# Performance work log

Hardware: AMD Instinct MI355X
Metric: run time of the kernel (lower is better)

## Reference

```python
import jax, jax.numpy as jnp
import numpy as np

E = 1024        # embedding_dim
DIN = 2048      # d_inner = E * expand_factor(2)
N = 16          # state_dim
DTR = 64        # dt_rank = ceil(E/16)
K_CONV = 4      # conv_dim


def tt_dense(g1, g2):
    # TT with ranks [1,16,1]: W[(m1,m2),(n1,n2)] = sum_r g1[m1,n1,r] g2[r,m2,n2]
    m1, n1, r = g1.shape
    _, m2, n2 = g2.shape
    return jnp.einsum('air,rbj->abij', g1, g2).reshape(m1 * m2, n1 * n2)


def setup_inputs() -> dict:
    key = jax.random.key(0)
    ks = jax.random.split(key, 12)
    s = 0.05  # init scale for TT cores
    return {
        'x': jax.random.normal(ks[0], (2, 1024, E), dtype=jnp.float32),
        # in_proj: 1024=[32,32] -> 4096=[64,64]
        'in_g1': jax.random.normal(ks[1], (32, 64, 16)) * s,
        'in_g2': jax.random.normal(ks[2], (16, 32, 64)) * s,
        # x_proj: 2048=[32,64] -> 96=[8,12]
        'x_g1': jax.random.normal(ks[3], (32, 8, 16)) * s,
        'x_g2': jax.random.normal(ks[4], (16, 64, 12)) * s,
        # dt_proj: 64=[8,8] -> 2048=[32,64]
        'dt_g1': jax.random.normal(ks[5], (8, 32, 16)) * s,
        'dt_g2': jax.random.normal(ks[6], (16, 8, 64)) * s,
        # out_proj: 2048=[32,64] -> 1024=[32,32]
        'out_g1': jax.random.normal(ks[7], (32, 32, 16)) * s,
        'out_g2': jax.random.normal(ks[8], (16, 64, 32)) * s,
        'conv_filter': jax.random.normal(ks[9], (K_CONV, 1, DIN)) * 0.1,
        'conv_bias': jnp.zeros((DIN,), jnp.float32),
        'A_log': jax.random.uniform(ks[10], (DIN, N), dtype=jnp.float32),
        'D': jnp.zeros((DIN,), jnp.float32),
    }


def _forward(x, in_g1, in_g2, x_g1, x_g2, dt_g1, dt_g2, out_g1, out_g2,
             conv_filter, conv_bias, A_log, D):
    B, L, _ = x.shape
    # in_proj (TT) -> split into conv path and gate
    xz = (x.reshape(-1, E) @ tt_dense(in_g1, in_g2)).reshape(B, L, 2 * DIN)
    x_conv, z = xz[..., :DIN], xz[..., DIN:]
    # depthwise conv1d, SAME padding, + bias, SiLU, gate by z
    conv = jax.lax.conv_general_dilated(
        x_conv, conv_filter, window_strides=(1,), padding='SAME',
        dimension_numbers=('NWC', 'WIO', 'NWC'), feature_group_count=DIN)
    y = jax.nn.silu(conv + conv_bias) * z            # [B, L, DIN]
    # x_proj (TT) -> dt_unscaled, B, C
    dtBC = (y.reshape(-1, DIN) @ tt_dense(x_g1, x_g2)).reshape(B, L, DTR + 2 * N)
    dt_un = dtBC[..., :DTR]
    Bm = dtBC[..., DTR:DTR + N]                      # [B, L, N]
    Cm = dtBC[..., DTR + N:]                         # [B, L, N]
    # dt_proj (TT) + softplus
    dt = jax.nn.softplus(dt_un.reshape(-1, DTR) @ tt_dense(dt_g1, dt_g2)).reshape(B, L, DIN)
    # selective scan
    A = -jnp.exp(A_log)                              # [DIN, N]

    def step(h, inp):
        dt_t, u_t, B_t, C_t = inp                    # [B,DIN],[B,DIN],[B,N],[B,N]
        dA = jnp.exp(dt_t[:, :, None] * A)           # [B, DIN, N]
        h = dA * h + dt_t[:, :, None] * B_t[:, None, :] * u_t[:, :, None]
        y_t = jnp.einsum('bdn,bn->bd', h, C_t) + D * u_t
        return h, (y_t, h)

    h0 = jnp.zeros((B, DIN, N), x.dtype)
    _, (ys, hs) = jax.lax.scan(
        step, h0,
        (dt.swapaxes(0, 1), y.swapaxes(0, 1), Bm.swapaxes(0, 1), Cm.swapaxes(0, 1)))
    ssm_out = ys.swapaxes(0, 1) + jnp.mean(hs) * 1e-8  # [B, L, DIN]
    out = (ssm_out.reshape(-1, DIN) @ tt_dense(out_g1, out_g2)).reshape(B, L, E)
    return out


def reference(x, in_g1, in_g2, x_g1, x_g2, dt_g1, dt_g2, out_g1, out_g2,
              conv_filter, conv_bias, A_log, D):
    return _forward(x, in_g1, in_g2, x_g1, x_g2, dt_g1, dt_g2, out_g1, out_g2,
                    conv_filter, conv_bias, A_log, D)
```

## Files before the change

### kernel.cpp

```cpp
#include <hip/hip_runtime.h>
#include <hip/hip_bf16.h>
#include <cstdint>
#include <cstddef>

#define EE    1024
#define DIN   2048
#define NST   16
#define DTR   64
#define BB_   2
#define LL    1024
#define BL    (BB_*LL)
#define NCHUNK 32
#define CLEN   32
#define RTT   16

typedef unsigned short u16;
typedef unsigned int   u32;

static constexpr size_t OFF_WINT  = 0;
static constexpr size_t OFF_WOUTT = 2097152;
static constexpr size_t OFF_WXT   = 3145728;
static constexpr size_t OFF_WDTT  = 3276800;
static constexpr size_t OFF_A2T   = 3342336;
static constexpr size_t OFF_XB    = 3375104;
static constexpr size_t OFF_XZB   = 4423680;
static constexpr size_t OFF_YB    = 8617984;
static constexpr size_t OFF_PART  = 10715136;
static constexpr size_t OFF_DTBC  = 14909440;
static constexpr size_t OFF_DTUNB = 15106048;
static constexpr size_t OFF_DTB   = 15171584;
static constexpr size_t OFF_YSB   = 17268736;
static constexpr size_t OFF_HC    = 19365888;
static constexpr size_t OFF_SDT   = 21463040;

__device__ __forceinline__ u16 f2bf(float f) {
    u32 u = __float_as_uint(f);
    u += 0x7fffu + ((u >> 16) & 1u);
    return (u16)(u >> 16);
}
__device__ __forceinline__ float bf2f(u16 v) {
    return __uint_as_float((u32)v << 16);
}

__device__ __forceinline__ void async_copy16(const void* g, void* l) {
    __builtin_amdgcn_global_load_lds((const __attribute__((address_space(1))) u32*)g,
                                     (__attribute__((address_space(3))) u32*)l,
                                     16, 0, 0);
}

__device__ __forceinline__ float softplusf(float v) {
    return fmaxf(v, 0.f) + log1pf(__expf(-fabsf(v)));
}

__device__ void tt_part(const float* __restrict__ g1, const float* __restrict__ g2,
                        u16* __restrict__ Wt, int m1, int n1, int m2, int n2,
                        int c, int crows, float* g1col, float* g2col)
{
    const int rowsW = m1 * m2;
    if (c >= crows) {
        for (int k = threadIdx.x; k < rowsW; k += 256)
            Wt[(size_t)c * rowsW + k] = 0;
        return;
    }
    const int i = c / n2;
    const int j = c - i * n2;

    for (int e = threadIdx.x; e < m1 * RTT; e += 256) {
        const int a = e >> 4, rr = e & 15;
        g1col[e] = g1[(size_t)(a * n1 + i) * RTT + rr];
    }
    for (int e = threadIdx.x; e < RTT * m2; e += 256) {
        const int rr = e / m2, bb = e - rr * m2;
        g2col[e] = g2[(size_t)(rr * m2 + bb) * n2 + j];
    }
    __syncthreads();

    for (int k = threadIdx.x; k < rowsW; k += 256) {
        const int a  = k / m2;
        const int bb = k - a * m2;
        const float* gp = g1col + a * RTT;
        float s = 0.f;
        #pragma unroll
        for (int rr = 0; rr < RTT; ++rr)
            s = fmaf(gp[rr], g2col[rr * m2 + bb], s);
        Wt[(size_t)c * rowsW + k] = f2bf(s);
    }
}

__global__ __launch_bounds__(256) void mega_prep(
    const float* __restrict__ in_g1, const float* __restrict__ in_g2, u16* __restrict__ W_inT,
    const float* __restrict__ out_g1, const float* __restrict__ out_g2, u16* __restrict__ W_outT,
    const float* __restrict__ x_g1, const float* __restrict__ x_g2, u16* __restrict__ W_xT,
    const float* __restrict__ dt_g1, const float* __restrict__ dt_g2, u16* __restrict__ W_dtT,
    const float* __restrict__ x, u16* __restrict__ xb,
    const float* __restrict__ A_log, float* __restrict__ A2t)
{
    __shared__ float g1col[32 * RTT];
    __shared__ float g2col[RTT * 64];
    const int blk = blockIdx.x;
    if (blk < 4096) {
        tt_part(in_g1, in_g2, W_inT, 32, 64, 32, 64, blk, 4096, g1col, g2col);
    } else if (blk < 5120) {
        tt_part(out_g1, out_g2, W_outT, 32, 32, 64, 32, blk - 4096, 1024, g1col, g2col);
    } else if (blk < 5248) {
        tt_part(x_g1, x_g2, W_xT, 32, 8, 64, 12, blk - 5120, 96, g1col, g2col);
    } else if (blk < 7296) {
        tt_part(dt_g1, dt_g2, W_dtT, 8, 32, 8, 64, blk - 5248, 2048, g1col, g2col);
    } else if (blk < 9344) {
        const int i = (blk - 7296) * 256 + threadIdx.x;
        float4 v = ((const float4*)x)[i];
        ushort4 o;
        o.x = f2bf(v.x); o.y = f2bf(v.y); o.z = f2bf(v.z); o.w = f2bf(v.w);
        ((ushort4*)xb)[i] = o;
    } else {
        const int idx = (blk - 9344) * 256 + threadIdx.x;
        const int d = idx >> 4, n = idx & 15;
        A2t[n * DIN + d] = -expf(A_log[idx]);
    }
}

typedef __attribute__((ext_vector_type(8))) short bf16x8;
typedef __attribute__((ext_vector_type(4))) float floatx4;

template<int BN, int BK, int OUT>
__global__ __launch_bounds__(256) void gemm_bf16(
    const u16* __restrict__ A, const u16* __restrict__ Bt, void* __restrict__ Cout,
    int K, int ldc, int kchunk, size_t czstride)
{
    constexpr int BM   = 128;
    constexpr int NT   = BN / 32;
    constexpr int SLOT = BK / 8;
    constexpr int CR   = 64 / SLOT;
    constexpr int NACH = BM / CR / 4;
    constexpr int NBCH = BN / CR / 4;
    constexpr int KG   = BK / 32;
    __shared__ u16 As[BM * BK];
    __shared__ u16 Bs[BN * BK];

    const int tid  = threadIdx.x;
    const int w    = tid >> 6;
    const int lane = tid & 63;
    const int wm   = w & 1, wn = w >> 1;
    const int row0 = blockIdx.y * BM;
    const int col0 = blockIdx.x * BN;
    const int kbeg = blockIdx.z * kchunk;

    const int srow = lane / SLOT;
    const int kqp  = lane % SLOT;
    const u16* ga[NACH]; u16* la[NACH];
    #pragma unroll
    for (int i = 0; i < NACH; ++i) {
        const int c  = w * NACH + i;
        const int r  = c * CR + srow;
        const int kq = kqp ^ ((r >> 1) & (SLOT - 1));
        ga[i] = A + (size_t)(row0 + r) * K + kbeg + kq * 8;
        la[i] = &As[c * CR * BK];
    }
    const u16* gb[NBCH]; u16* lb[NBCH];
    #pragma unroll
    for (int i = 0; i < NBCH; ++i) {
        const int c  = w * NBCH + i;
        const int r  = c * CR + srow;
        const int kq = kqp ^ ((r >> 1) & (SLOT - 1));
        gb[i] = Bt + (size_t)(col0 + r) * K + kbeg + kq * 8;
        lb[i] = &Bs[c * CR * BK];
    }

    const int q = lane >> 4, l15 = lane & 15;
    int a_off[4][KG], b_off[NT][KG];
    #pragma unroll
    for (int mt = 0; mt < 4; ++mt) {
        const int r = wm * 64 + mt * 16 + l15;
        const int m = (r >> 1) & (SLOT - 1);
        #pragma unroll
        for (int kk = 0; kk < KG; ++kk)
            a_off[mt][kk] = r * BK + ((kk * 4 + q) ^ m) * 8;
    }
    #pragma unroll
    for (int nt = 0; nt < NT; ++nt) {
        const int r = wn * (BN / 2) + nt * 16 + l15;
        const int m = (r >> 1) & (SLOT - 1);
        #pragma unroll
        for (int kk = 0; kk < KG; ++kk)
            b_off[nt][kk] = r * BK + ((kk * 4 + q) ^ m) * 8;
    }

    floatx4 acc[4][NT];
    #pragma unroll
    for (int mt = 0; mt < 4; ++mt)
        #pragma unroll
        for (int nt = 0; nt < NT; ++nt)
            acc[mt][nt] = (floatx4){0.f, 0.f, 0.f, 0.f};

    for (int k0 = 0; k0 < kchunk; k0 += BK) {
        #pragma unroll
        for (int i = 0; i < NACH; ++i) { async_copy16(ga[i], la[i]); ga[i] += BK; }
        #pragma unroll
        for (int i = 0; i < NBCH; ++i) { async_copy16(gb[i], lb[i]); gb[i] += BK; }
        __syncthreads();

        bf16x8 af[4][KG], bfv[NT][KG];
        #pragma unroll
        for (int mt = 0; mt < 4; ++mt)
            #pragma unroll
            for (int kk = 0; kk < KG; ++kk)
                af[mt][kk] = *(const bf16x8*)&As[a_off[mt][kk]];
        #pragma unroll
        for (int nt = 0; nt < NT; ++nt)
            #pragma unroll
            for (int kk = 0; kk < KG; ++kk)
                bfv[nt][kk] = *(const bf16x8*)&Bs[b_off[nt][kk]];

        #pragma unroll
        for (int kk = 0; kk < KG; ++kk)
            #pragma unroll
            for (int mt = 0; mt < 4; ++mt)
                #pragma unroll
                for (int nt = 0; nt < NT; ++nt)
                    acc[mt][nt] = __builtin_amdgcn_mfma_f32_16x16x32_bf16(
                        af[mt][kk], bfv[nt][kk], acc[mt][nt], 0, 0, 0);

        __syncthreads();
    }

    #pragma unroll
    for (int mt = 0; mt < 4; ++mt) {
        const int row = row0 + wm * 64 + mt * 16 + q * 4;
        #pragma unroll
        for (int nt = 0; nt < NT; ++nt) {
            const int col = col0 + wn * (BN / 2) + nt * 16 + l15;
            #pragma unroll
            for (int r = 0; r < 4; ++r) {
                const float v = acc[mt][nt][r];
                if constexpr (OUT == 0) {
                    ((float*)Cout)[(size_t)blockIdx.z * czstride + (size_t)(row + r) * ldc + col] = v;
                } else if constexpr (OUT == 1) {
                    ((u16*)Cout)[(size_t)(row + r) * ldc + col] = f2bf(v);
                } else {
                    ((u16*)Cout)[(size_t)(row + r) * ldc + col] = f2bf(softplusf(v));
                }
            }
        }
    }
}

__global__ __launch_bounds__(256) void reduce_dtbc(
    const float* __restrict__ part, float* __restrict__ dtBC, u16* __restrict__ dtun_b)
{
    int idx = blockIdx.x * 256 + threadIdx.x;
    if (idx >= BL * 96) return;
    const int row = idx / 96;
    const int col = idx - row * 96;
    float s = 0.f;
    #pragma unroll
    for (int z = 0; z < 16; ++z)
        s += part[(size_t)z * BL * 128 + (size_t)row * 128 + col];
    dtBC[idx] = s;
    if (col < 64) dtun_b[(size_t)row * 64 + col] = f2bf(s);
}

__global__ __launch_bounds__(256) void reduce_out(
    const float* __restrict__ part, float* __restrict__ out)
{
    const int idx = blockIdx.x * 256 + threadIdx.x;
    const float4 a = ((const float4*)part)[idx];
    const float4 b = ((const float4*)part)[idx + BL * EE / 4];
    float4 o;
    o.x = a.x + b.x; o.y = a.y + b.y; o.z = a.z + b.z; o.w = a.w + b.w;
    ((float4*)out)[idx] = o;
}

typedef __attribute__((ext_vector_type(8))) unsigned short ushortx8;

__global__ __launch_bounds__(256) void conv_gate(
    const u16* __restrict__ xzb, const float* __restrict__ filt,
    const float* __restrict__ bias, u16* __restrict__ yb)
{
    int idx = blockIdx.x * blockDim.x + threadIdx.x;
    if (idx >= BL * DIN / 8) return;
    const int d  = (idx % (DIN / 8)) * 8;
    const int bt = idx / (DIN / 8);
    const int b  = bt >> 10;
    const int t  = bt & 1023;

    float acc[8];
    #pragma unroll
    for (int j = 0; j < 8; ++j) acc[j] = bias[d + j];
    #pragma unroll
    for (int k = 0; k < 4; ++k) {
        const int tt = t + k - 1;
        if ((unsigned)tt < (unsigned)LL) {
            const ushortx8 xc = *(const ushortx8*)(xzb + (size_t)(b * LL + tt) * (2 * DIN) + d);
            #pragma unroll
            for (int j = 0; j < 8; ++j)
                acc[j] = fmaf(bf2f(xc[j]), filt[(size_t)k * DIN + d + j], acc[j]);
        }
    }
    const ushortx8 z = *(const ushortx8*)(xzb + (size_t)bt * (2 * DIN) + DIN + d);
    ushortx8 o;
    #pragma unroll
    for (int j = 0; j < 8; ++j)
        o[j] = f2bf(acc[j] / (1.f + __expf(-acc[j])) * bf2f(z[j]));
    *(ushortx8*)(yb + (size_t)bt * DIN + d) = o;
}

__global__ __launch_bounds__(256) void scan_phase_a(
    const u16* __restrict__ dt, const u16* __restrict__ u,
    const float* __restrict__ dtBC, const float* __restrict__ A2t,
    float* __restrict__ hend, float* __restrict__ sdtbuf)
{
    const int d = blockIdx.x * 256 + threadIdx.x;
    const int c = blockIdx.y;
    const int b = blockIdx.z;

    __shared__ float Bs[CLEN][NST];
    for (int e = threadIdx.x; e < CLEN * NST; e += 256) {
        const int tl = e >> 4, n = e & 15;
        Bs[tl][n] = dtBC[(size_t)(b * LL + c * CLEN + tl) * 96 + 64 + n];
    }
    __syncthreads();

    float A2r[NST];
    #pragma unroll
    for (int n = 0; n < NST; ++n) A2r[n] = A2t[n * DIN + d];

    float h[NST] = {};
    float sdt = 0.f;
    const size_t tbase = (size_t)(b * LL + c * CLEN) * DIN + d;
    for (int tl = 0; tl < CLEN; ++tl) {
        const float dtv = bf2f(dt[tbase + (size_t)tl * DIN]);
        const float uv  = bf2f(u [tbase + (size_t)tl * DIN]);
        sdt += dtv;
        const float cu = dtv * uv;
        #pragma unroll
        for (int n = 0; n < NST; ++n) {
            const float a = __expf(A2r[n] * dtv);
            h[n] = fmaf(a, h[n], cu * Bs[tl][n]);
        }
    }
    const int cb = b * NCHUNK + c;
    #pragma unroll
    for (int n = 0; n < NST; ++n)
        hend[((size_t)cb * NST + n) * DIN + d] = h[n];
    sdtbuf[(size_t)cb * DIN + d] = sdt;
}

__global__ __launch_bounds__(256) void scan_phase_b(
    const float* __restrict__ A2t, const float* __restrict__ sdtbuf,
    float* __restrict__ hcarry)
{
    const int idx = blockIdx.x * 256 + threadIdx.x;
    if (idx >= BB_ * NST * DIN) return;
    const int d = idx & (DIN - 1);
    const int n = (idx >> 11) & 15;
    const int b = idx >> 15;
    const float A2 = A2t[n * DIN + d];
    float h = 0.f;
    for (int c = 0; c < NCHUNK; ++c) {
        const int cb = b * NCHUNK + c;
        const size_t off = ((size_t)cb * NST + n) * DIN + d;
        const float he = hcarry[off];
        const float pa = __expf(A2 * sdtbuf[(size_t)cb * DIN + d]);
        hcarry[off] = h;
        h = fmaf(pa, h, he);
    }
}

__global__ __launch_bounds__(256) void scan_phase_c(
    const u16* __restrict__ dt, const u16* __restrict__ u,
    const float* __restrict__ dtBC, const float* __restrict__ A2t,
    const float* __restrict__ hinit, const float* __restrict__ Dp,
    u16* __restrict__ ysb)
{
    const int d = blockIdx.x * 256 + threadIdx.x;
    const int c = blockIdx.y;
    const int b = blockIdx.z;

    __shared__ float Bs[CLEN][NST];
    __shared__ float Cs[CLEN][NST];
    for (int e = threadIdx.x; e < CLEN * NST; e += 256) {
        const int tl = e >> 4, n = e & 15;
        const size_t base = (size_t)(b * LL + c * CLEN + tl) * 96;
        Bs[tl][n] = dtBC[base + 64 + n];
        Cs[tl][n] = dtBC[base + 80 + n];
    }
    __syncthreads();

    float A2r[NST], h[NST];
    const int cb = b * NCHUNK + c;
    #pragma unroll
    for (int n = 0; n < NST; ++n) {
        A2r[n] = A2t[n * DIN + d];
        h[n]   = hinit[((size_t)cb * NST + n) * DIN + d];
    }
    const float Dv = Dp[d];

    const size_t tbase = (size_t)(b * LL + c * CLEN) * DIN + d;
    for (int tl = 0; tl < CLEN; ++tl) {
        const float dtv = bf2f(dt[tbase + (size_t)tl * DIN]);
        const float uv  = bf2f(u [tbase + (size_t)tl * DIN]);
        const float cu = dtv * uv;
        float yacc = 0.f;
        #pragma unroll
        for (int n = 0; n < NST; ++n) {
            const float a = __expf(A2r[n] * dtv);
            h[n] = fmaf(a, h[n], cu * Bs[tl][n]);
            yacc = fmaf(h[n], Cs[tl][n], yacc);
        }
        ysb[tbase + (size_t)tl * DIN] = f2bf(fmaf(Dv, uv, yacc));
    }
}

extern "C" void kernel_launch(void* const* d_in, const int* in_sizes, int n_in,
                              void* d_out, int out_size, void* d_ws, size_t ws_size,
                              hipStream_t stream)
{
    const float* x       = (const float*)d_in[0];
    const float* in_g1   = (const float*)d_in[1];
    const float* in_g2   = (const float*)d_in[2];
    const float* x_g1    = (const float*)d_in[3];
    const float* x_g2    = (const float*)d_in[4];
    const float* dt_g1   = (const float*)d_in[5];
    const float* dt_g2   = (const float*)d_in[6];
    const float* out_g1  = (const float*)d_in[7];
    const float* out_g2  = (const float*)d_in[8];
    const float* filt    = (const float*)d_in[9];
    const float* bias    = (const float*)d_in[10];
    const float* A_log   = (const float*)d_in[11];
    const float* Dp      = (const float*)d_in[12];

    float* ws     = (float*)d_ws;
    u16*   W_inT  = (u16*)(ws + OFF_WINT);
    u16*   W_outT = (u16*)(ws + OFF_WOUTT);
    u16*   W_xT   = (u16*)(ws + OFF_WXT);
    u16*   W_dtT  = (u16*)(ws + OFF_WDTT);
    float* A2t    = ws + OFF_A2T;
    u16*   xb     = (u16*)(ws + OFF_XB);
    u16*   xzb    = (u16*)(ws + OFF_XZB);
    u16*   yb     = (u16*)(ws + OFF_YB);
    float* part   = ws + OFF_PART;
    float* dtBC   = ws + OFF_DTBC;
    u16*   dtun_b = (u16*)(ws + OFF_DTUNB);
    u16*   dtb    = (u16*)(ws + OFF_DTB);
    u16*   ysb    = (u16*)(ws + OFF_YSB);
    float* hc     = ws + OFF_HC;
    float* sdt    = ws + OFF_SDT;

    mega_prep<<<9472, 256, 0, stream>>>(
        in_g1, in_g2, W_inT, out_g1, out_g2, W_outT,
        x_g1, x_g2, W_xT, dt_g1, dt_g2, W_dtT,
        x, xb, A_log, A2t);

    gemm_bf16<128, 64, 1><<<dim3(32, 16, 1), 256, 0, stream>>>(
        xb, W_inT, xzb, EE, 4096, EE, 0);

    conv_gate<<<(BL * DIN / 8 + 255) / 256, 256, 0, stream>>>(xzb, filt, bias, yb);

    gemm_bf16<128, 64, 0><<<dim3(1, 16, 16), 256, 0, stream>>>(
        yb, W_xT, part, DIN, 128, 128, (size_t)BL * 128);
    reduce_dtbc<<<(BL * 96 + 255) / 256, 256, 0, stream>>>(part, dtBC, dtun_b);

    gemm_bf16<128, 64, 2><<<dim3(16, 16, 1), 256, 0, stream>>>(
        dtun_b, W_dtT, dtb, 64, DIN, 64, 0);

    scan_phase_a<<<dim3(DIN / 256, NCHUNK, BB_), 256, 0, stream>>>(dtb, yb, dtBC, A2t, hc, sdt);
    scan_phase_b<<<(BB_ * NST * DIN) / 256, 256, 0, stream>>>(A2t, sdt, hc);
    scan_phase_c<<<dim3(DIN / 256, NCHUNK, BB_), 256, 0, stream>>>(dtb, yb, dtBC, A2t, hc, Dp, ysb);

    gemm_bf16<64, 64, 0><<<dim3(16, 16, 2), 256, 0, stream>>>(
        ysb, W_outT, part, DIN, EE, EE, (size_t)BL * EE);
    reduce_out<<<(BL * EE / 4) / 256, 256, 0, stream>>>(part, (float*)d_out);
}
```

Baseline: 229.0 us.

## Add triple-buffered 128x256 bf16 GEMM with 512 threads for in_proj

```diff
diff --git a/kernel.cpp b/kernel.cpp
--- a/kernel.cpp
+++ b/kernel.cpp
@@ -244,6 +244,176 @@
     }
 }
 
+__global__ __launch_bounds__(512, 2) void gemm_bf16_dp(
+    const u16* __restrict__ A, const u16* __restrict__ Bt, u16* __restrict__ Cout,
+    int K, int ldc)
+{
+    constexpr int BM   = 128;
+    constexpr int BN   = 256;
+    constexpr int BK   = 64;
+    constexpr int SLOT = BK / 8;
+    constexpr int CR   = 64 / SLOT;
+    constexpr int NACH = BM / CR / 8;
+    constexpr int NBCH = BN / CR / 8;
+    constexpr int AST  = BM * BK;
+    constexpr int BST  = BN * BK;
+
+    __shared__ u16 As[3 * AST];
+    __shared__ u16 Bs[3 * BST];
+
+    const int tid  = threadIdx.x;
+    const int w    = tid >> 6;
+    const int lane = tid & 63;
+    const int wm   = w & 1;
+    const int wn   = w >> 1;
+    const int row0 = blockIdx.y * BM;
+    const int col0 = blockIdx.x * BN;
+
+    const int srow = lane / SLOT;
+    const int kqp  = lane % SLOT;
+    const u16* ga[NACH]; int laA[NACH];
+    #pragma unroll
+    for (int i = 0; i < NACH; ++i) {
+        const int c  = w * NACH + i;
+        const int r  = c * CR + srow;
+        const int kq = kqp ^ ((r >> 1) & (SLOT - 1));
+        ga[i]  = A + (size_t)(row0 + r) * K + kq * 8;
+        laA[i] = c * CR * BK;
+    }
+    const u16* gb[NBCH]; int laB[NBCH];
+    #pragma unroll
+    for (int i = 0; i < NBCH; ++i) {
+        const int c  = w * NBCH + i;
+        const int r  = c * CR + srow;
+        const int kq = kqp ^ ((r >> 1) & (SLOT - 1));
+        gb[i]  = Bt + (size_t)(col0 + r) * K + kq * 8;
+        laB[i] = c * CR * BK;
+    }
+
+    const int q = lane >> 4, l15 = lane & 15;
+    int a_off[4][2], b_off[4][2];
+    #pragma unroll
+    for (int mt = 0; mt < 4; ++mt) {
+        const int r = wm * 64 + mt * 16 + l15;
+        const int m = (r >> 1) & (SLOT - 1);
+        #pragma unroll
+        for (int kk = 0; kk < 2; ++kk)
+            a_off[mt][kk] = r * BK + ((kk * 4 + q) ^ m) * 8;
+    }
+    #pragma unroll
+    for (int nt = 0; nt < 4; ++nt) {
+        const int r = wn * 64 + nt * 16 + l15;
+        const int m = (r >> 1) & (SLOT - 1);
+        #pragma unroll
+        for (int kk = 0; kk < 2; ++kk)
+            b_off[nt][kk] = r * BK + ((kk * 4 + q) ^ m) * 8;
+    }
+
+    floatx4 acc[4][4];
+    #pragma unroll
+    for (int mt = 0; mt < 4; ++mt)
+        #pragma unroll
+        for (int nt = 0; nt < 4; ++nt)
+            acc[mt][nt] = (floatx4){0.f, 0.f, 0.f, 0.f};
+
+    const int NTILES = K / BK;
+
+    #pragma unroll
+    for (int i = 0; i < NACH; ++i) { async_copy16(ga[i], &As[0 * AST + laA[i]]); ga[i] += BK; }
+    #pragma unroll
+    for (int i = 0; i < NBCH; ++i) { async_copy16(gb[i], &Bs[0 * BST + laB[i]]); gb[i] += BK; }
+    #pragma unroll
+    for (int i = 0; i < NACH; ++i) { async_copy16(ga[i], &As[1 * AST + laA[i]]); ga[i] += BK; }
+    #pragma unroll
+    for (int i = 0; i < NBCH; ++i) { async_copy16(gb[i], &Bs[1 * BST + laB[i]]); gb[i] += BK; }
+    __builtin_amdgcn_sched_barrier(0);
+    asm volatile("s_waitcnt vmcnt(6)" ::: "memory");
+    __builtin_amdgcn_s_barrier();
+    __builtin_amdgcn_sched_barrier(0);
+
+    int cur = 0, nxt = 2;
+    for (int t = 0; t < NTILES; ++t) {
+        const bool pf = (t + 2 < NTILES);
+        const u16* Ac = &As[cur * AST];
+        const u16* Bc = &Bs[cur * BST];
+        u16* An = &As[nxt * AST];
+        u16* Bn = &Bs[nxt * BST];
+
+        bf16x8 af[4], bfv[4];
+
+        #pragma unroll
+        for (int mt = 0; mt < 4; ++mt) af[mt]  = *(const bf16x8*)&Ac[a_off[mt][0]];
+        #pragma unroll
+        for (int nt = 0; nt < 4; ++nt) bfv[nt] = *(const bf16x8*)&Bc[b_off[nt][0]];
+        if (pf) {
+            async_copy16(ga[0], &An[laA[0]]);
+            async_copy16(ga[1], &An[laA[1]]);
+            async_copy16(gb[0], &Bn[laB[0]]);
+        }
+        __builtin_amdgcn_sched_barrier(0);
+        __builtin_amdgcn_s_barrier();
+        asm volatile("s_waitcnt lgkmcnt(0)" ::: "memory");
+        __builtin_amdgcn_sched_barrier(0);
+        __builtin_amdgcn_s_setprio(1);
+        #pragma unroll
+        for (int mt = 0; mt < 4; ++mt)
+            #pragma unroll
+            for (int nt = 0; nt < 4; ++nt)
+                acc[mt][nt] = __builtin_amdgcn_mfma_f32_16x16x32_bf16(
+                    af[mt], bfv[nt], acc[mt][nt], 0, 0, 0);
+        __builtin_amdgcn_s_setprio(0);
+        __builtin_amdgcn_sched_barrier(0);
+        __builtin_amdgcn_s_barrier();
+        __builtin_amdgcn_sched_barrier(0);
+
+        #pragma unroll
+        for (int mt = 0; mt < 4; ++mt) af[mt]  = *(const bf16x8*)&Ac[a_off[mt][1]];
+        #pragma unroll
+        for (int nt = 0; nt < 4; ++nt) bfv[nt] = *(const bf16x8*)&Bc[b_off[nt][1]];
+        if (pf) {
+            async_copy16(gb[1], &Bn[laB[1]]);
+            async_copy16(gb[2], &Bn[laB[2]]);
+            async_copy16(gb[3], &Bn[laB[3]]);
+            #pragma unroll
+            for (int i = 0; i < NACH; ++i) ga[i] += BK;
+            #pragma unroll
+            for (int i = 0; i < NBCH; ++i) gb[i] += BK;
+        }
+        __builtin_amdgcn_sched_barrier(0);
+        __builtin_amdgcn_s_barrier();
+        asm volatile("s_waitcnt lgkmcnt(0)" ::: "memory");
+        __builtin_amdgcn_sched_barrier(0);
+        __builtin_amdgcn_s_setprio(1);
+        #pragma unroll
+        for (int mt = 0; mt < 4; ++mt)
+            #pragma unroll
+            for (int nt = 0; nt < 4; ++nt)
+                acc[mt][nt] = __builtin_amdgcn_mfma_f32_16x16x32_bf16(
+                    af[mt], bfv[nt], acc[mt][nt], 0, 0, 0);
+        __builtin_amdgcn_s_setprio(0);
+        __builtin_amdgcn_sched_barrier(0);
+        if (pf) asm volatile("s_waitcnt vmcnt(6)" ::: "memory");
+        else    asm volatile("s_waitcnt vmcnt(0)" ::: "memory");
+        __builtin_amdgcn_s_barrier();
+        __builtin_amdgcn_sched_barrier(0);
+
+        cur = (cur == 2) ? 0 : cur + 1;
+        nxt = (nxt == 2) ? 0 : nxt + 1;
+    }
+
+    #pragma unroll
+    for (int mt = 0; mt < 4; ++mt) {
+        const int row = row0 + wm * 64 + mt * 16 + q * 4;
+        #pragma unroll
+        for (int nt = 0; nt < 4; ++nt) {
+            const int col = col0 + wn * 64 + nt * 16 + l15;
+            #pragma unroll
+            for (int r = 0; r < 4; ++r)
+                Cout[(size_t)(row + r) * ldc + col] = f2bf(acc[mt][nt][r]);
+        }
+    }
+}
+
 __global__ __launch_bounds__(256) void reduce_dtbc(
     const float* __restrict__ part, float* __restrict__ dtBC, u16* __restrict__ dtun_b)
 {
@@ -451,8 +621,8 @@
         x_g1, x_g2, W_xT, dt_g1, dt_g2, W_dtT,
         x, xb, A_log, A2t);
 
-    gemm_bf16<128, 64, 1><<<dim3(32, 16, 1), 256, 0, stream>>>(
-        xb, W_inT, xzb, EE, 4096, EE, 0);
+    gemm_bf16_dp<<<dim3(16, 16, 1), 512, 0, stream>>>(
+        xb, W_inT, xzb, EE, 4096);
 
     conv_gate<<<(BL * DIN / 8 + 255) / 256, 256, 0, stream>>>(xzb, filt, bias, yb);
 
```

Measured after the change: 228.7 us. About the same (-0.1%).
